# Kernel optimization log

Hardware: AMD Instinct MI355X
Metric: run time of the kernel (lower is better)

The kernel has to match this reference:

```python
import jax, jax.numpy as jnp
import numpy as np

PHI = 0.1  # fraction of pruned weights randomized per inference


def setup_inputs() -> dict:
    key = jax.random.key(0)
    k1, k2, k3 = jax.random.split(key, 3)
    d_out, d_in, batch = 8192, 8192, 256
    W = jax.random.normal(k1, (d_out, d_in), jnp.float32) * 0.02
    prune = jax.random.uniform(k2, (d_out, d_in)) < 0.9
    W = jnp.where(prune, 0.0, W)
    mask = (W == 0.0)  # _register_masks: pruned positions
    x = jax.random.normal(k3, (batch, d_in), jnp.float32)
    return {"x": x, "W": W, "mask": mask}


def reference(x, W, mask):
    # --- _apply_random_flip (vectorized) ---
    n_pruned = int(np.asarray(jnp.sum(mask)))          # concrete mask -> static count
    n_flip = max(1, int(PHI * n_pruned))
    keep = ~mask
    n_keep = jnp.sum(keep).astype(W.dtype)
    wk = jnp.where(keep, W, 0.0)
    mean = jnp.sum(wk) / n_keep
    # torch .std() is unbiased (n-1 denominator)
    var = jnp.sum(jnp.where(keep, (W - mean) ** 2, 0.0)) / (n_keep - 1.0)
    std = jnp.sqrt(var)
    key = jax.random.key(42)
    ks, kv = jax.random.split(key)
    # uniform random permutation of pruned indices -> top_k of random scores
    scores = jnp.where(mask.ravel(), jax.random.uniform(ks, (W.size,)), -1.0)
    _, flip_idx = jax.lax.top_k(scores, n_flip)        # [n_flip] flat indices into W
    vals = jax.random.normal(kv, (n_flip,), W.dtype) * std * 0.1
    W_flipped = W.ravel().at[flip_idx].set(vals).reshape(W.shape)
    # --- base_model forward (Linear, no bias) ---
    out = x @ W_flipped.T                               # [batch, d_out]
    # --- _restore_masks: zero flipped weights again (no effect on out) ---
    _ = jnp.where(mask, 0.0, W_flipped)
    return out
```

## Files before the change

kernel.cpp:

```cpp
#include <hip/hip_runtime.h>

typedef unsigned int u32;
typedef unsigned long long u64;
typedef unsigned short u16;

#define NTOT   67108864u
#define T0P    7399424u
#define PBASE  14452u
#define NSUP   1932u
#define NWSEG  4096u
#define WCAP   2176u
#define RCAP   4352u
#define KSPLIT 8
#define RBLK   512u
#define SEGPB  8

struct Scalars {
  double sumW;
  double sumW2;
  u64 npruned;
  u64 nflip;
  float stdf;
  float pad;
};

#define OFF_COLSUM 0ull
#define OFF_ALLOC  8192ull
#define OFF_SBASE  16384ull
#define OFF_SC     24576ull
#define OFF_SEGCNT 24704ull
#define OFF_BHIST  41216ull
#define OFF_BDEST  4235520ull
#define OFF_XBF    8429824ull
#define OFF_SEGS   12624128ull
#define OFF_ROUTED 48275712ull
#define OFF_WBF    81846400ull
#define WS_NEED_WBF 216064128ull
#define ROUTED_CAP 8388608u
#define OFF_OUTP   OFF_SEGS

__host__ __device__ inline void tf2x32(u32 k0, u32 k1, u32 x0, u32 x1, u32& y0, u32& y1) {
  u32 ks2 = k0 ^ k1 ^ 0x1BD11BDAu;
  x0 += k0; x1 += k1;
#define TFR(r) { x0 += x1; x1 = (x1 << (r)) | (x1 >> (32 - (r))); x1 ^= x0; }
  TFR(13) TFR(15) TFR(26) TFR(6)  x0 += k1;  x1 += ks2 + 1u;
  TFR(17) TFR(29) TFR(16) TFR(24) x0 += ks2; x1 += k0 + 2u;
  TFR(13) TFR(15) TFR(26) TFR(6)  x0 += k0;  x1 += k1 + 3u;
  TFR(17) TFR(29) TFR(16) TFR(24) x0 += k1;  x1 += ks2 + 4u;
  TFR(13) TFR(15) TFR(26) TFR(6)  x0 += ks2; x1 += k0 + 5u;
#undef TFR
  y0 = x0; y1 = x1;
}

__device__ inline u32 jax_bits32(u32 k0, u32 k1, u32 i) {
  u32 y0, y1; tf2x32(k0, k1, 0u, i, y0, y1);
  return y0 ^ y1;
}

__device__ inline u16 f2bf(float f) {
  union { float f; u32 u; } c; c.f = f;
  u32 r = ((c.u >> 16) & 1u) + 0x7FFFu;
  return (u16)((c.u + r) >> 16);
}

__device__ inline float erfinv32(float x) {
  float w = -log1pf(-x * x);
  float p;
  if (w < 5.0f) {
    w -= 2.5f;
    p = 2.81022636e-08f;
    p = fmaf(p, w, 3.43273939e-07f);
    p = fmaf(p, w, -3.5233877e-06f);
    p = fmaf(p, w, -4.39150654e-06f);
    p = fmaf(p, w, 0.00021858087f);
    p = fmaf(p, w, -0.00125372503f);
    p = fmaf(p, w, -0.00417768164f);
    p = fmaf(p, w, 0.246640727f);
    p = fmaf(p, w, 1.50140941f);
  } else {
    w = sqrtf(w) - 3.0f;
    p = -0.000200214257f;
    p = fmaf(p, w, 0.000100950558f);
    p = fmaf(p, w, 0.00134934322f);
    p = fmaf(p, w, -0.00367342844f);
    p = fmaf(p, w, 0.00573950773f);
    p = fmaf(p, w, -0.0076224613f);
    p = fmaf(p, w, 0.00943887047f);
    p = fmaf(p, w, 1.00167406f);
    p = fmaf(p, w, 2.83297682f);
  }
  return p * x;
}

__device__ inline void pass1_half(const float* __restrict__ W, Scalars* sc,
                                  u32* segcnt, u32* segs, u32 uk0, u32 uk1,
                                  u32 bid, u32 t, u32 lo, u32 hi, bool first) {
  u32 gid = bid * 256 + t;
  u32 lane = t & 63;
  u32 wid = gid >> 6;
  u32* wseg = segs + (u64)wid * WCAP;
  u32 wbase = first ? 0u : segcnt[wid];
  float sf = 0.f, sf2 = 0.f; u32 cnt = 0;
  const u32 stride4 = 1024u * 256u * 4u;
  for (u32 b4 = lo + gid * 4; b4 < hi; b4 += stride4) {
    float4 w4 = *(const float4*)(W + b4);
    u32 sb0 = jax_bits32(uk0, uk1, b4 + 0) >> 9;
    u32 sb1 = jax_bits32(uk0, uk1, b4 + 1) >> 9;
    u32 sb2 = jax_bits32(uk0, uk1, b4 + 2) >> 9;
    u32 sb3 = jax_bits32(uk0, uk1, b4 + 3) >> 9;
    float we[4] = {w4.x, w4.y, w4.z, w4.w};
    u32 sbv[4] = {sb0, sb1, sb2, sb3};
    u32 cand[4]; u32 nc = 0;
#pragma unroll
    for (int e = 0; e < 4; e++) {
      float w = we[e];
      sf += w;
      sf2 = fmaf(w, w, sf2);
      bool pr = (w == 0.0f);
      cnt += pr ? 1u : 0u;
      if (pr && sbv[e] >= T0P) { cand[nc] = b4 + e; nc++; }
    }
    u32 inc = nc;
#pragma unroll
    for (int o = 1; o < 64; o <<= 1) { u32 v = (u32)__shfl_up((int)inc, o); if (lane >= (u32)o) inc += v; }
    u32 tot = (u32)__shfl((int)inc, 63);
    u32 pos = wbase + inc - nc;
    for (u32 k2 = 0; k2 < nc; k2++)
      if (pos + k2 < WCAP) wseg[pos + k2] = cand[k2];
    wbase += tot;
  }
  double s = (double)sf, s2 = (double)sf2;
  for (int o = 32; o > 0; o >>= 1) {
    s += __shfl_down(s, o); s2 += __shfl_down(s2, o); cnt += __shfl_down(cnt, o);
  }
  if (lane == 0) {
    atomicAdd(&sc->sumW, s);
    atomicAdd(&sc->sumW2, s2);
    atomicAdd(&sc->npruned, (u64)cnt);
    segcnt[wid] = first ? wbase : ((wbase > WCAP) ? WCAP : wbase);
  }
}

__device__ inline void wconv_range(const float* __restrict__ W, u16* __restrict__ wbf,
                                   u32 i0, u32 glo, u32 ghi) {
  const u32 stride = 512u * 256u;
  for (u32 g = glo + i0; g < ghi; g += stride) {
    const float4* p = (const float4*)(W + (u64)g * 8);
    float4 a = p[0], b = p[1];
    uint4 o;
    o.x = (u32)f2bf(a.x) | ((u32)f2bf(a.y) << 16);
    o.y = (u32)f2bf(a.z) | ((u32)f2bf(a.w) << 16);
    o.z = (u32)f2bf(b.x) | ((u32)f2bf(b.y) << 16);
    o.w = (u32)f2bf(b.z) | ((u32)f2bf(b.w) << 16);
    *(uint4*)(wbf + (u64)g * 8) = o;
  }
}

__global__ __launch_bounds__(256) void k_pass1wA(const float* __restrict__ W,
                                                 u16* __restrict__ wbf,
                                                 const float* __restrict__ x,
                                                 u16* __restrict__ xbf,
                                                 Scalars* sc, u32* segcnt, u32* segs,
                                                 u32 uk0, u32 uk1, u32 dowbf) {
  u32 t = threadIdx.x, bid = blockIdx.x;
  if (bid < 1024u) {
    pass1_half(W, sc, segcnt, segs, uk0, uk1, bid, t, 0u, NTOT / 2u, true);
  } else if (bid < 1536u) {
    if (dowbf) wconv_range(W, wbf, (bid - 1024u) * 256 + t, 0u, NTOT / 16u);
  } else {
    u32 i0 = (bid - 1536u) * 256 + t;
    const u32 stride = 512u * 256u;
    for (u32 g = i0; g < 524288u; g += stride) {
      float4 v = ((const float4*)x)[g];
      ushort4 o; o.x = f2bf(v.x); o.y = f2bf(v.y); o.z = f2bf(v.z); o.w = f2bf(v.w);
      ((ushort4*)xbf)[g] = o;
    }
  }
}

__global__ __launch_bounds__(256) void k_pass1wB(const float* __restrict__ W,
                                                 u16* __restrict__ wbf,
                                                 Scalars* sc, u32* segcnt, u32* segs,
                                                 u32 uk0, u32 uk1) {
  u32 t = threadIdx.x, bid = blockIdx.x;
  if (bid < 1024u) {
    pass1_half(W, sc, segcnt, segs, uk0, uk1, bid, t, NTOT / 2u, NTOT, false);
  } else {
    wconv_range(W, wbf, (bid - 1024u) * 256 + t, NTOT / 16u, NTOT / 8u);
  }
}

__global__ __launch_bounds__(256) void k_route_a(const u32* __restrict__ segs,
                                                 const u32* __restrict__ segcnt,
                                                 u32* bhist, u32 uk0, u32 uk1) {
  __shared__ u32 lhist[2048];
  u32 t = threadIdx.x;
  for (u32 j = t; j < 2048; j += 256) lhist[j] = 0;
  __syncthreads();
#pragma unroll 1
  for (int sg = 0; sg < SEGPB; sg++) {
    u32 wid = blockIdx.x * SEGPB + sg;
    u32 n = segcnt[wid]; if (n > WCAP) n = WCAP;
    const u32* sp = segs + (u64)wid * WCAP;
    for (u32 i = t; i < n; i += 256) {
      u32 sup = (jax_bits32(uk0, uk1, sp[i]) >> 18) - PBASE;
      atomicAdd(&lhist[sup], 1u);
    }
  }
  __syncthreads();
  for (u32 j = t; j < 2048; j += 256) bhist[blockIdx.x * 2048 + j] = lhist[j];
}

__global__ __launch_bounds__(256) void k_colscan(const u32* __restrict__ bhist,
                                                 u32* bdest, u32* colsum) {
  __shared__ u32 wtmp[4];
  u32 s = blockIdx.x, t = threadIdx.x, lane = t & 63, wv = t >> 6;
  u32 v0 = bhist[(t * 2 + 0) * 2048 + s];
  u32 v1 = bhist[(t * 2 + 1) * 2048 + s];
  u32 pr = v0 + v1;
  u32 inc = pr;
#pragma unroll
  for (int o = 1; o < 64; o <<= 1) { u32 x = (u32)__shfl_up((int)inc, o); if (lane >= (u32)o) inc += x; }
  if (lane == 63) wtmp[wv] = inc;
  __syncthreads();
  u32 woff = 0;
  for (u32 w = 0; w < wv; w++) woff += wtmp[w];
  u32 base = woff + inc - pr;
  bdest[(t * 2 + 0) * 2048 + s] = base;
  bdest[(t * 2 + 1) * 2048 + s] = base + v0;
  if (t == 255) colsum[s] = woff + inc;
}

__global__ __launch_bounds__(256) void k_scan(const u32* __restrict__ colsum, Scalars* sc,
                                              u32* alloc, u32* sbase) {
  __shared__ u32 h[2048];
  __shared__ u32 wtmp[4];
  u32 t = threadIdx.x, lane = t & 63, wv = t >> 6;
  for (u32 j = t; j < 2048; j += 256) h[j] = colsum[j];
  __syncthreads();
  {
    u32 a[8]; u32 s8 = 0;
#pragma unroll
    for (int k = 0; k < 8; k++) { a[k] = h[t * 8 + k]; s8 += a[k]; }
    u32 inc = s8;
#pragma unroll
    for (int o = 1; o < 64; o <<= 1) { u32 v = (u32)__shfl_up((int)inc, o); if (lane >= (u32)o) inc += v; }
    if (lane == 63) wtmp[wv] = inc;
    __syncthreads();
    u32 woff = 0; for (u32 w = 0; w < wv; w++) woff += wtmp[w];
    u32 base = woff + inc - s8;
#pragma unroll
    for (int k = 0; k < 8; k++) { alloc[t * 8 + k] = base; base += a[k]; }
    __syncthreads();
  }
  {
    u32 a[8]; u32 s8 = 0;
#pragma unroll
    for (int k = 0; k < 8; k++) { a[k] = h[2047 - (t * 8 + k)]; s8 += a[k]; }
    u32 inc = s8;
#pragma unroll
    for (int o = 1; o < 64; o <<= 1) { u32 v = (u32)__shfl_up((int)inc, o); if (lane >= (u32)o) inc += v; }
    if (lane == 63) wtmp[wv] = inc;
    __syncthreads();
    u32 woff = 0; for (u32 w = 0; w < wv; w++) woff += wtmp[w];
    u32 base = woff + inc - s8;
#pragma unroll
    for (int k = 0; k < 8; k++) { sbase[2047 - (t * 8 + k)] = base; base += a[k]; }
  }
  if (t == 0) {
    double nk = (double)NTOT - (double)sc->npruned;
    double mean = sc->sumW / nk;
    double var = (sc->sumW2 - 2.0 * mean * sc->sumW + nk * mean * mean) / (nk - 1.0);
    sc->stdf = (float)sqrt(var);
    u64 nfi = (u64)(0.1 * (double)sc->npruned);
    if (nfi < 1) nfi = 1;
    sc->nflip = nfi;
  }
}

__global__ __launch_bounds__(256) void k_route_b(const u32* __restrict__ segs,
                                                 const u32* __restrict__ segcnt,
                                                 const u32* __restrict__ alloc,
                                                 const u32* __restrict__ bdest,
                                                 u32* routed, u32 uk0, u32 uk1) {
  __shared__ u32 lcur[2048];
  u32 t = threadIdx.x;
  for (u32 j = t; j < 2048; j += 256) lcur[j] = alloc[j] + bdest[blockIdx.x * 2048 + j];
  __syncthreads();
#pragma unroll 1
  for (int sg = 0; sg < SEGPB; sg++) {
    u32 wid = blockIdx.x * SEGPB + sg;
    u32 n = segcnt[wid]; if (n > WCAP) n = WCAP;
    const u32* sp = segs + (u64)wid * WCAP;
    for (u32 i = t; i < n; i += 256) {
      u32 idx = sp[i];
      u32 sup = (jax_bits32(uk0, uk1, idx) >> 18) - PBASE;
      u32 pos = atomicAdd(&lcur[sup], 1u);
      if (pos < ROUTED_CAP) routed[pos] = idx;
    }
  }
}

__device__ inline void suf512(const u32* cnt, u32* suf, u32* wtmp) {
  u32 t = threadIdx.x, lane = t & 63, wv = t >> 6;
  u32 a0 = cnt[511 - t * 2], a1 = cnt[510 - t * 2];
  u32 s = a0 + a1;
  u32 inc = s;
#pragma unroll
  for (int o = 1; o < 64; o <<= 1) { u32 v = (u32)__shfl_up((int)inc, o); if (lane >= (u32)o) inc += v; }
  if (lane == 63) wtmp[wv] = inc;
  __syncthreads();
  u32 woff = 0;
  for (u32 w = 0; w < wv; w++) woff += wtmp[w];
  u32 base = woff + inc - s;
  suf[511 - t * 2] = base;
  suf[510 - t * 2] = base + a0;
  __syncthreads();
}

template<int MODE>
__global__ __launch_bounds__(256) void k_rank(float* __restrict__ W,
                                              u16* __restrict__ wbf,
                                              const u32* __restrict__ colsum,
                                              const u32* __restrict__ alloc,
                                              const u32* __restrict__ sbase,
                                              const u32* __restrict__ routed,
                                              const Scalars* __restrict__ sc,
                                              u32 uk0, u32 uk1, u32 vk0, u32 vk1) {
  u32 p = blockIdx.x;
  u32 n = colsum[p]; if (n == 0) return;
  if (n > RCAP) n = RCAP;
  u64 nflip = sc->nflip;
  u32 rbase = sbase[p];
  if ((u64)rbase >= nflip) return;
  __shared__ u32 sIdx[RCAP];
  __shared__ u16 sFine[RCAP];
  __shared__ u32 pIdx[RCAP];
  __shared__ u32 hist[512], gbase[512], cur[512], wtmp[4];
  u32 t = threadIdx.x;
  for (u32 j = t; j < 512; j += 256) hist[j] = 0;
  __syncthreads();
  const u32* src = routed + alloc[p];
  for (u32 i = t; i < n; i += 256) {
    u32 idx = src[i];
    u32 f = (jax_bits32(uk0, uk1, idx) >> 9) & 511u;
    sIdx[i] = idx;
    sFine[i] = (u16)f;
    atomicAdd(&hist[f], 1u);
  }
  __syncthreads();
  suf512(hist, gbase, wtmp);
  for (u32 j = t; j < 512; j += 256) cur[j] = gbase[j];
  __syncthreads();
  for (u32 i = t; i < n; i += 256) {
    u32 pos = atomicAdd(&cur[sFine[i]], 1u);
    pIdx[pos] = sIdx[i];
  }
  __syncthreads();
  float stdf = sc->stdf;
  for (u32 i = t; i < n; i += 256) {
    u32 f = sFine[i];
    u32 g0 = gbase[f], g1 = g0 + hist[f];
    u32 v = sIdx[i];
    u32 ord = 0;
    for (u32 q = g0; q < g1; q++) ord += (pIdx[q] < v) ? 1u : 0u;
    u64 rank = (u64)rbase + g0 + ord;
    if (rank >= nflip) continue;
    u32 bits = jax_bits32(vk0, vk1, (u32)rank);
    union { u32 u; float fl; } cv; cv.u = 0x3F800000u | (bits >> 9);
    float fu = cv.fl - 1.0f;
    const float lo = -0.99999994f;
    float u2 = fmaxf(lo, fu * 2.0f + lo);
    float nrm = 1.41421354f * erfinv32(u2);
    float val = (nrm * stdf) * 0.1f;
    if (MODE == 1) wbf[v] = f2bf(val);
    else           W[v] = val;
  }
}

typedef __bf16 bf16x8 __attribute__((ext_vector_type(8)));
typedef float f32x4 __attribute__((ext_vector_type(4)));

__global__ __launch_bounds__(256, 3) void k_gemm2(const u16* __restrict__ xbf,
                                                  const u16* __restrict__ wbf,
                                                  float* __restrict__ outp) {
  __shared__ u16 As[128 * 64];
  __shared__ u16 Bs[128 * 64];
  u32 i = blockIdx.x;
  u32 xcd = i & 7u, slot = i >> 3;
  u32 mi = slot & 1u, qq = slot >> 1;
  u32 pid = xcd * 64u + qq;
  u32 kidx = pid >> 6;
  u32 nb = pid & 63u;
  u32 mrow = mi * 128u, nrow = nb * 128u;
  u32 kbase = kidx * 1024u;
  u32 tid = threadIdx.x;
  u32 lane = tid & 63, wv = tid >> 6;
  u32 l8 = lane & 7;
  u32 lr = lane >> 3;
  u32 wm = wv >> 1, wn = wv & 1;
  u32 r = lane & 15, q = lane >> 4;
  f32x4 acc[4][4];
#pragma unroll
  for (int a = 0; a < 4; a++)
#pragma unroll
    for (int b = 0; b < 4; b++) acc[a][b] = (f32x4){0.f, 0.f, 0.f, 0.f};

  for (u32 kb = kbase; kb < kbase + 1024u; kb += 64u) {
#pragma unroll
    for (int j = 0; j < 4; j++) {
      u32 g = wv * 4 + (u32)j;
      u32 row = g * 8 + lr;
      u32 sc = ((l8 ^ (row & 7u)) * 8u);
      const u16* ga = xbf + (u64)(mrow + row) * 8192 + kb + sc;
      __builtin_amdgcn_global_load_lds((const u32*)ga, (u32*)&As[g * 512u], 16, 0, 0);
      const u16* gb = wbf + (u64)(nrow + row) * 8192 + kb + sc;
      __builtin_amdgcn_global_load_lds((const u32*)gb, (u32*)&Bs[g * 512u], 16, 0, 0);
    }
    __syncthreads();
#pragma unroll
    for (int ks = 0; ks < 2; ks++) {
      bf16x8 a[4], b[4];
      u32 ch = (u32)(ks * 4) + q;
#pragma unroll
      for (int mt = 0; mt < 4; mt++) {
        u32 row = wm * 64 + (u32)mt * 16 + r;
        a[mt] = *(bf16x8*)&As[row * 64 + ((ch ^ (r & 7u)) * 8u)];
      }
#pragma unroll
      for (int nt = 0; nt < 4; nt++) {
        u32 row = wn * 64 + (u32)nt * 16 + r;
        b[nt] = *(bf16x8*)&Bs[row * 64 + ((ch ^ (r & 7u)) * 8u)];
      }
#pragma unroll
      for (int mt = 0; mt < 4; mt++)
#pragma unroll
        for (int nt = 0; nt < 4; nt++)
          acc[mt][nt] = __builtin_amdgcn_mfma_f32_16x16x32_bf16(a[mt], b[nt], acc[mt][nt], 0, 0, 0);
    }
    __syncthreads();
  }
  float* op = outp + (u64)kidx * 2097152u;
  u32 quad = lane >> 4, col = lane & 15;
#pragma unroll
  for (int mt = 0; mt < 4; mt++)
#pragma unroll
    for (int nt = 0; nt < 4; nt++) {
      u32 n = nrow + wn * 64 + (u32)nt * 16 + col;
#pragma unroll
      for (int rg = 0; rg < 4; rg++) {
        u32 m = mrow + wm * 64 + (u32)mt * 16 + quad * 4 + (u32)rg;
        op[(u64)m * 8192 + n] = acc[mt][nt][rg];
      }
    }
}

__global__ __launch_bounds__(256) void k_redout(const float* __restrict__ part,
                                                float* __restrict__ out) {
  u32 i = blockIdx.x * 256 + threadIdx.x;
  float4 s = ((const float4*)part)[i];
#pragma unroll
  for (int k = 1; k < KSPLIT; k++) {
    float4 v = ((const float4*)(part + (u64)k * 2097152u))[i];
    s.x += v.x; s.y += v.y; s.z += v.z; s.w += v.w;
  }
  ((float4*)out)[i] = s;
}

__global__ __launch_bounds__(256, 2) void k_gemm_fb(const u16* __restrict__ xbf,
                                                    const float* __restrict__ W,
                                                    float* __restrict__ out) {
  __shared__ u16 xs[256 * 72];
  __shared__ u16 wsm[64 * 72];
  u32 tid = threadIdx.x;
  u32 lane = tid & 63, wv = tid >> 6;
  u32 nt0 = blockIdx.x * 64;
  u32 kbase = blockIdx.y * 2048u;
  f32x4 acc[4][4];
#pragma unroll
  for (int i = 0; i < 4; i++)
#pragma unroll
    for (int j = 0; j < 4; j++) acc[i][j] = (f32x4){0.f, 0.f, 0.f, 0.f};
  for (u32 kb = kbase; kb < kbase + 2048u; kb += 64u) {
#pragma unroll
    for (int r8 = 0; r8 < 8; r8++) {
      u32 row = r8 * 32 + (tid >> 3);
      u32 kseg = (tid & 7) * 8;
      uint4 v = *(const uint4*)(xbf + (u64)row * 8192 + kb + kseg);
      *(uint4*)&xs[row * 72 + kseg] = v;
    }
#pragma unroll
    for (int rr = 0; rr < 4; rr++) {
      u32 f4 = rr * 256 + tid;
      u32 row = f4 >> 4;
      u32 kc = (f4 & 15) * 4;
      float4 v = *(const float4*)(W + (u64)(nt0 + row) * 8192 + kb + kc);
      ushort4 o; o.x = f2bf(v.x); o.y = f2bf(v.y); o.z = f2bf(v.z); o.w = f2bf(v.w);
      *(ushort4*)&wsm[row * 72 + kc] = o;
    }
    __syncthreads();
#pragma unroll
    for (int ks = 0; ks < 2; ks++) {
      bf16x8 a[4], b[4];
      u32 koff = ks * 32 + (lane >> 4) * 8;
      u32 rsel = lane & 15;
#pragma unroll
      for (int mt = 0; mt < 4; mt++) a[mt] = *(bf16x8*)&xs[(wv * 64 + mt * 16 + rsel) * 72 + koff];
#pragma unroll
      for (int nt = 0; nt < 4; nt++) b[nt] = *(bf16x8*)&wsm[(nt * 16 + rsel) * 72 + koff];
#pragma unroll
      for (int mt = 0; mt < 4; mt++)
#pragma unroll
        for (int nt = 0; nt < 4; nt++)
          acc[mt][nt] = __builtin_amdgcn_mfma_f32_16x16x32_bf16(a[mt], b[nt], acc[mt][nt], 0, 0, 0);
    }
    __syncthreads();
  }
  u32 quad = lane >> 4, col = lane & 15;
#pragma unroll
  for (int mt = 0; mt < 4; mt++)
#pragma unroll
    for (int nt = 0; nt < 4; nt++) {
      u32 n = nt0 + nt * 16 + col;
#pragma unroll
      for (int rg = 0; rg < 4; rg++) {
        u32 m = wv * 64 + mt * 16 + quad * 4 + rg;
        atomicAdd(&out[(u64)m * 8192 + n], acc[mt][nt][rg]);
      }
    }
}

extern "C" void kernel_launch(void* const* d_in, const int* in_sizes, int n_in,
                              void* d_out, int out_size, void* d_ws, size_t ws_size,
                              hipStream_t stream) {
  const float* x; float* W;
  if (in_sizes[0] == 2097152) { x = (const float*)d_in[0]; W = (float*)d_in[1]; }
  else                        { x = (const float*)d_in[1]; W = (float*)d_in[0]; }
  float* out = (float*)d_out;
  char* ws = (char*)d_ws;

  u32* colsum = (u32*)(ws + OFF_COLSUM);
  u32* alloc  = (u32*)(ws + OFF_ALLOC);
  u32* sbase  = (u32*)(ws + OFF_SBASE);
  Scalars* sc = (Scalars*)(ws + OFF_SC);
  u32* segcnt = (u32*)(ws + OFF_SEGCNT);
  u32* bhist  = (u32*)(ws + OFF_BHIST);
  u32* bdest  = (u32*)(ws + OFF_BDEST);
  u16* xbf    = (u16*)(ws + OFF_XBF);
  u32* segs   = (u32*)(ws + OFF_SEGS);
  u32* routed = (u32*)(ws + OFF_ROUTED);
  u16* wbf    = (u16*)(ws + OFF_WBF);
  float* outp = (float*)(ws + OFF_OUTP);

  bool t1 = (ws_size >= (size_t)WS_NEED_WBF);

  u32 a0, a1, b0, b1;
  tf2x32(0u, 42u, 0u, 0u, a0, a1);
  tf2x32(0u, 42u, 0u, 1u, b0, b1);

  hipMemsetAsync(sc, 0, sizeof(Scalars), stream);

  k_pass1wA<<<2048, 256, 0, stream>>>(W, wbf, x, xbf, sc, segcnt, segs, a0, a1, t1 ? 1u : 0u);
  k_pass1wB<<<t1 ? 1536 : 1024, 256, 0, stream>>>(W, wbf, sc, segcnt, segs, a0, a1);
  k_route_a<<<RBLK, 256, 0, stream>>>(segs, segcnt, bhist, a0, a1);
  k_colscan<<<2048, 256, 0, stream>>>(bhist, bdest, colsum);
  k_scan<<<1, 256, 0, stream>>>(colsum, sc, alloc, sbase);
  k_route_b<<<RBLK, 256, 0, stream>>>(segs, segcnt, alloc, bdest, routed, a0, a1);
  if (t1) {
    k_rank<1><<<NSUP, 256, 0, stream>>>(W, wbf, colsum, alloc, sbase, routed, sc, a0, a1, b0, b1);
    k_gemm2<<<1024, 256, 0, stream>>>(xbf, wbf, outp);
    k_redout<<<2048, 256, 0, stream>>>(outp, out);
  } else {
    k_rank<0><<<NSUP, 256, 0, stream>>>(W, wbf, colsum, alloc, sbase, routed, sc, a0, a1, b0, b1);
    hipMemsetAsync(out, 0, (size_t)out_size * 4, stream);
    dim3 g(128, 4);
    k_gemm_fb<<<g, 256, 0, stream>>>(xbf, W, out);
  }
}
```

Before: 1.134 ms.

## Fuse routing, scan and rank stages into one cooperative persistent kernel

The five middle kernels (histogram, column scan, global scan, scatter route, rank/flip) are merged into a single cooperative kernel of 768 blocks that uses grid-wide syncs between phases, with a shared-memory union covering all phases. The two-pass weight statistics/conversion kernels are also merged into one launch over the full array, with the bf16 conversion given more blocks. The aim is to remove launch gaps and tail effects between many short dependent kernels. The cost is grid-sync overhead and fewer blocks working on the rank phase, where each block now loops over several super-buckets.

```diff
diff --git a/kernel.cpp b/kernel.cpp
--- a/kernel.cpp
+++ b/kernel.cpp
@@ -1,4 +1,7 @@
 #include <hip/hip_runtime.h>
+#include <hip/hip_cooperative_groups.h>
+
+namespace cg = cooperative_groups;
 
 typedef unsigned int u32;
 typedef unsigned long long u64;
@@ -12,8 +15,7 @@
 #define WCAP   2176u
 #define RCAP   4352u
 #define KSPLIT 8
-#define RBLK   512u
-#define SEGPB  8
+#define MBLK   768u
 
 struct Scalars {
   double sumW;
@@ -30,12 +32,12 @@
 #define OFF_SC     24576ull
 #define OFF_SEGCNT 24704ull
 #define OFF_BHIST  41216ull
-#define OFF_BDEST  4235520ull
-#define OFF_XBF    8429824ull
-#define OFF_SEGS   12624128ull
-#define OFF_ROUTED 48275712ull
-#define OFF_WBF    81846400ull
-#define WS_NEED_WBF 216064128ull
+#define OFF_BDEST  8429824ull
+#define OFF_XBF    16818432ull
+#define OFF_SEGS   21012736ull
+#define OFF_ROUTED 56664320ull
+#define OFF_WBF    90218752ull
+#define WS_NEED_WBF 224436480ull
 #define ROUTED_CAP 8388608u
 #define OFF_OUTP   OFF_SEGS
 
@@ -92,84 +94,76 @@
   return p * x;
 }
 
-__device__ inline void pass1_half(const float* __restrict__ W, Scalars* sc,
-                                  u32* segcnt, u32* segs, u32 uk0, u32 uk1,
-                                  u32 bid, u32 t, u32 lo, u32 hi, bool first) {
-  u32 gid = bid * 256 + t;
-  u32 lane = t & 63;
-  u32 wid = gid >> 6;
-  u32* wseg = segs + (u64)wid * WCAP;
-  u32 wbase = first ? 0u : segcnt[wid];
-  float sf = 0.f, sf2 = 0.f; u32 cnt = 0;
-  const u32 stride4 = 1024u * 256u * 4u;
-  for (u32 b4 = lo + gid * 4; b4 < hi; b4 += stride4) {
-    float4 w4 = *(const float4*)(W + b4);
-    u32 sb0 = jax_bits32(uk0, uk1, b4 + 0) >> 9;
-    u32 sb1 = jax_bits32(uk0, uk1, b4 + 1) >> 9;
-    u32 sb2 = jax_bits32(uk0, uk1, b4 + 2) >> 9;
-    u32 sb3 = jax_bits32(uk0, uk1, b4 + 3) >> 9;
-    float we[4] = {w4.x, w4.y, w4.z, w4.w};
-    u32 sbv[4] = {sb0, sb1, sb2, sb3};
-    u32 cand[4]; u32 nc = 0;
-#pragma unroll
-    for (int e = 0; e < 4; e++) {
-      float w = we[e];
-      sf += w;
-      sf2 = fmaf(w, w, sf2);
-      bool pr = (w == 0.0f);
-      cnt += pr ? 1u : 0u;
-      if (pr && sbv[e] >= T0P) { cand[nc] = b4 + e; nc++; }
-    }
-    u32 inc = nc;
-#pragma unroll
-    for (int o = 1; o < 64; o <<= 1) { u32 v = (u32)__shfl_up((int)inc, o); if (lane >= (u32)o) inc += v; }
-    u32 tot = (u32)__shfl((int)inc, 63);
-    u32 pos = wbase + inc - nc;
-    for (u32 k2 = 0; k2 < nc; k2++)
-      if (pos + k2 < WCAP) wseg[pos + k2] = cand[k2];
-    wbase += tot;
-  }
-  double s = (double)sf, s2 = (double)sf2;
-  for (int o = 32; o > 0; o >>= 1) {
-    s += __shfl_down(s, o); s2 += __shfl_down(s2, o); cnt += __shfl_down(cnt, o);
-  }
-  if (lane == 0) {
-    atomicAdd(&sc->sumW, s);
-    atomicAdd(&sc->sumW2, s2);
-    atomicAdd(&sc->npruned, (u64)cnt);
-    segcnt[wid] = first ? wbase : ((wbase > WCAP) ? WCAP : wbase);
-  }
-}
-
-__device__ inline void wconv_range(const float* __restrict__ W, u16* __restrict__ wbf,
-                                   u32 i0, u32 glo, u32 ghi) {
-  const u32 stride = 512u * 256u;
-  for (u32 g = glo + i0; g < ghi; g += stride) {
-    const float4* p = (const float4*)(W + (u64)g * 8);
-    float4 a = p[0], b = p[1];
-    uint4 o;
-    o.x = (u32)f2bf(a.x) | ((u32)f2bf(a.y) << 16);
-    o.y = (u32)f2bf(a.z) | ((u32)f2bf(a.w) << 16);
-    o.z = (u32)f2bf(b.x) | ((u32)f2bf(b.y) << 16);
-    o.w = (u32)f2bf(b.z) | ((u32)f2bf(b.w) << 16);
-    *(uint4*)(wbf + (u64)g * 8) = o;
-  }
-}
-
-__global__ __launch_bounds__(256) void k_pass1wA(const float* __restrict__ W,
-                                                 u16* __restrict__ wbf,
-                                                 const float* __restrict__ x,
-                                                 u16* __restrict__ xbf,
-                                                 Scalars* sc, u32* segcnt, u32* segs,
-                                                 u32 uk0, u32 uk1, u32 dowbf) {
-  u32 t = threadIdx.x, bid = blockIdx.x;
+__global__ __launch_bounds__(256) void k_pass1w(const float* __restrict__ W,
+                                                u16* __restrict__ wbf,
+                                                const float* __restrict__ x,
+                                                u16* __restrict__ xbf,
+                                                Scalars* sc, u32* segcnt, u32* segs,
+                                                u32 uk0, u32 uk1, u32 dowbf) {
+  u32 t = threadIdx.x;
+  u32 bid = blockIdx.x;
   if (bid < 1024u) {
-    pass1_half(W, sc, segcnt, segs, uk0, uk1, bid, t, 0u, NTOT / 2u, true);
-  } else if (bid < 1536u) {
-    if (dowbf) wconv_range(W, wbf, (bid - 1024u) * 256 + t, 0u, NTOT / 16u);
+    u32 gid = bid * 256 + t;
+    u32 lane = t & 63;
+    u32 wid = gid >> 6;
+    u32* wseg = segs + (u64)wid * WCAP;
+    u32 wbase = 0;
+    float sf = 0.f, sf2 = 0.f; u32 cnt = 0;
+    const u32 stride4 = 1024u * 256u * 4u;
+    for (u32 b4 = gid * 4; b4 < NTOT; b4 += stride4) {
+      float4 w4 = *(const float4*)(W + b4);
+      u32 sb0 = jax_bits32(uk0, uk1, b4 + 0) >> 9;
+      u32 sb1 = jax_bits32(uk0, uk1, b4 + 1) >> 9;
+      u32 sb2 = jax_bits32(uk0, uk1, b4 + 2) >> 9;
+      u32 sb3 = jax_bits32(uk0, uk1, b4 + 3) >> 9;
+      float we[4] = {w4.x, w4.y, w4.z, w4.w};
+      u32 sbv[4] = {sb0, sb1, sb2, sb3};
+      u32 cand[4]; u32 nc = 0;
+#pragma unroll
+      for (int e = 0; e < 4; e++) {
+        float w = we[e];
+        sf += w;
+        sf2 = fmaf(w, w, sf2);
+        bool pr = (w == 0.0f);
+        cnt += pr ? 1u : 0u;
+        if (pr && sbv[e] >= T0P) { cand[nc] = b4 + e; nc++; }
+      }
+      u32 inc = nc;
+#pragma unroll
+      for (int o = 1; o < 64; o <<= 1) { u32 v = (u32)__shfl_up((int)inc, o); if (lane >= (u32)o) inc += v; }
+      u32 tot = (u32)__shfl((int)inc, 63);
+      u32 pos = wbase + inc - nc;
+      for (u32 k2 = 0; k2 < nc; k2++)
+        if (pos + k2 < WCAP) wseg[pos + k2] = cand[k2];
+      wbase += tot;
+    }
+    double s = (double)sf, s2 = (double)sf2;
+    for (int o = 32; o > 0; o >>= 1) {
+      s += __shfl_down(s, o); s2 += __shfl_down(s2, o); cnt += __shfl_down(cnt, o);
+    }
+    if (lane == 0) {
+      atomicAdd(&sc->sumW, s);
+      atomicAdd(&sc->sumW2, s2);
+      atomicAdd(&sc->npruned, (u64)cnt);
+      segcnt[wid] = (wbase > WCAP) ? WCAP : wbase;
+    }
+  } else if (bid < 1984u) {
+    if (!dowbf) return;
+    u32 i0 = (bid - 1024u) * 256 + t;
+    const u32 stride = 960u * 256u;
+    for (u32 g = i0; g < NTOT / 8u; g += stride) {
+      const float4* p = (const float4*)(W + (u64)g * 8);
+      float4 a = p[0], b = p[1];
+      uint4 o;
+      o.x = (u32)f2bf(a.x) | ((u32)f2bf(a.y) << 16);
+      o.y = (u32)f2bf(a.z) | ((u32)f2bf(a.w) << 16);
+      o.z = (u32)f2bf(b.x) | ((u32)f2bf(b.y) << 16);
+      o.w = (u32)f2bf(b.z) | ((u32)f2bf(b.w) << 16);
+      *(uint4*)(wbf + (u64)g * 8) = o;
+    }
   } else {
-    u32 i0 = (bid - 1536u) * 256 + t;
-    const u32 stride = 512u * 256u;
+    u32 i0 = (bid - 1984u) * 256 + t;
+    const u32 stride = 64u * 256u;
     for (u32 g = i0; g < 524288u; g += stride) {
       float4 v = ((const float4*)x)[g];
       ushort4 o; o.x = f2bf(v.x); o.y = f2bf(v.y); o.z = f2bf(v.z); o.w = f2bf(v.w);
@@ -178,128 +172,13 @@
   }
 }
 
-__global__ __launch_bounds__(256) void k_pass1wB(const float* __restrict__ W,
-                                                 u16* __restrict__ wbf,
-                                                 Scalars* sc, u32* segcnt, u32* segs,
-                                                 u32 uk0, u32 uk1) {
-  u32 t = threadIdx.x, bid = blockIdx.x;
-  if (bid < 1024u) {
-    pass1_half(W, sc, segcnt, segs, uk0, uk1, bid, t, NTOT / 2u, NTOT, false);
-  } else {
-    wconv_range(W, wbf, (bid - 1024u) * 256 + t, NTOT / 16u, NTOT / 8u);
-  }
-}
-
-__global__ __launch_bounds__(256) void k_route_a(const u32* __restrict__ segs,
-                                                 const u32* __restrict__ segcnt,
-                                                 u32* bhist, u32 uk0, u32 uk1) {
-  __shared__ u32 lhist[2048];
-  u32 t = threadIdx.x;
-  for (u32 j = t; j < 2048; j += 256) lhist[j] = 0;
-  __syncthreads();
-#pragma unroll 1
-  for (int sg = 0; sg < SEGPB; sg++) {
-    u32 wid = blockIdx.x * SEGPB + sg;
-    u32 n = segcnt[wid]; if (n > WCAP) n = WCAP;
-    const u32* sp = segs + (u64)wid * WCAP;
-    for (u32 i = t; i < n; i += 256) {
-      u32 sup = (jax_bits32(uk0, uk1, sp[i]) >> 18) - PBASE;
-      atomicAdd(&lhist[sup], 1u);
-    }
-  }
-  __syncthreads();
-  for (u32 j = t; j < 2048; j += 256) bhist[blockIdx.x * 2048 + j] = lhist[j];
-}
-
-__global__ __launch_bounds__(256) void k_colscan(const u32* __restrict__ bhist,
-                                                 u32* bdest, u32* colsum) {
-  __shared__ u32 wtmp[4];
-  u32 s = blockIdx.x, t = threadIdx.x, lane = t & 63, wv = t >> 6;
-  u32 v0 = bhist[(t * 2 + 0) * 2048 + s];
-  u32 v1 = bhist[(t * 2 + 1) * 2048 + s];
-  u32 pr = v0 + v1;
-  u32 inc = pr;
-#pragma unroll
-  for (int o = 1; o < 64; o <<= 1) { u32 x = (u32)__shfl_up((int)inc, o); if (lane >= (u32)o) inc += x; }
-  if (lane == 63) wtmp[wv] = inc;
-  __syncthreads();
-  u32 woff = 0;
-  for (u32 w = 0; w < wv; w++) woff += wtmp[w];
-  u32 base = woff + inc - pr;
-  bdest[(t * 2 + 0) * 2048 + s] = base;
-  bdest[(t * 2 + 1) * 2048 + s] = base + v0;
-  if (t == 255) colsum[s] = woff + inc;
-}
-
-__global__ __launch_bounds__(256) void k_scan(const u32* __restrict__ colsum, Scalars* sc,
-                                              u32* alloc, u32* sbase) {
-  __shared__ u32 h[2048];
-  __shared__ u32 wtmp[4];
-  u32 t = threadIdx.x, lane = t & 63, wv = t >> 6;
-  for (u32 j = t; j < 2048; j += 256) h[j] = colsum[j];
-  __syncthreads();
-  {
-    u32 a[8]; u32 s8 = 0;
-#pragma unroll
-    for (int k = 0; k < 8; k++) { a[k] = h[t * 8 + k]; s8 += a[k]; }
-    u32 inc = s8;
-#pragma unroll
-    for (int o = 1; o < 64; o <<= 1) { u32 v = (u32)__shfl_up((int)inc, o); if (lane >= (u32)o) inc += v; }
-    if (lane == 63) wtmp[wv] = inc;
-    __syncthreads();
-    u32 woff = 0; for (u32 w = 0; w < wv; w++) woff += wtmp[w];
-    u32 base = woff + inc - s8;
-#pragma unroll
-    for (int k = 0; k < 8; k++) { alloc[t * 8 + k] = base; base += a[k]; }
-    __syncthreads();
-  }
-  {
-    u32 a[8]; u32 s8 = 0;
-#pragma unroll
-    for (int k = 0; k < 8; k++) { a[k] = h[2047 - (t * 8 + k)]; s8 += a[k]; }
-    u32 inc = s8;
-#pragma unroll
-    for (int o = 1; o < 64; o <<= 1) { u32 v = (u32)__shfl_up((int)inc, o); if (lane >= (u32)o) inc += v; }
-    if (lane == 63) wtmp[wv] = inc;
-    __syncthreads();
-    u32 woff = 0; for (u32 w = 0; w < wv; w++) woff += wtmp[w];
-    u32 base = woff + inc - s8;
-#pragma unroll
-    for (int k = 0; k < 8; k++) { sbase[2047 - (t * 8 + k)] = base; base += a[k]; }
-  }
-  if (t == 0) {
-    double nk = (double)NTOT - (double)sc->npruned;
-    double mean = sc->sumW / nk;
-    double var = (sc->sumW2 - 2.0 * mean * sc->sumW + nk * mean * mean) / (nk - 1.0);
-    sc->stdf = (float)sqrt(var);
-    u64 nfi = (u64)(0.1 * (double)sc->npruned);
-    if (nfi < 1) nfi = 1;
-    sc->nflip = nfi;
-  }
-}
-
-__global__ __launch_bounds__(256) void k_route_b(const u32* __restrict__ segs,
-                                                 const u32* __restrict__ segcnt,
-                                                 const u32* __restrict__ alloc,
-                                                 const u32* __restrict__ bdest,
-                                                 u32* routed, u32 uk0, u32 uk1) {
-  __shared__ u32 lcur[2048];
-  u32 t = threadIdx.x;
-  for (u32 j = t; j < 2048; j += 256) lcur[j] = alloc[j] + bdest[blockIdx.x * 2048 + j];
-  __syncthreads();
-#pragma unroll 1
-  for (int sg = 0; sg < SEGPB; sg++) {
-    u32 wid = blockIdx.x * SEGPB + sg;
-    u32 n = segcnt[wid]; if (n > WCAP) n = WCAP;
-    const u32* sp = segs + (u64)wid * WCAP;
-    for (u32 i = t; i < n; i += 256) {
-      u32 idx = sp[i];
-      u32 sup = (jax_bits32(uk0, uk1, idx) >> 18) - PBASE;
-      u32 pos = atomicAdd(&lcur[sup], 1u);
-      if (pos < ROUTED_CAP) routed[pos] = idx;
-    }
-  }
-}
+union MidLds {
+  struct { u32 lhist[2048]; } ra;
+  struct { u32 wt[4]; } cb;
+  struct { u32 h[2048]; u32 wt[4]; } cs;
+  struct { u32 lcur[2048]; } rb;
+  struct { u32 pIdx[RCAP]; u16 sFine[RCAP]; u32 hist[512]; u32 gbase[512]; u32 cur[512]; u32 wt[4]; } rk;
+};
 
 __device__ inline void suf512(const u32* cnt, u32* suf, u32* wtmp) {
   u32 t = threadIdx.x, lane = t & 63, wv = t >> 6;
@@ -319,62 +198,152 @@
 }
 
 template<int MODE>
-__global__ __launch_bounds__(256) void k_rank(float* __restrict__ W,
-                                              u16* __restrict__ wbf,
-                                              const u32* __restrict__ colsum,
-                                              const u32* __restrict__ alloc,
-                                              const u32* __restrict__ sbase,
-                                              const u32* __restrict__ routed,
-                                              const Scalars* __restrict__ sc,
-                                              u32 uk0, u32 uk1, u32 vk0, u32 vk1) {
-  u32 p = blockIdx.x;
-  u32 n = colsum[p]; if (n == 0) return;
-  if (n > RCAP) n = RCAP;
+__global__ __launch_bounds__(256, 3) void k_mid(const u32* __restrict__ segs,
+                                                const u32* __restrict__ segcnt,
+                                                u32* bhist, u32* bdest,
+                                                u32* colsum, u32* alloc, u32* sbase,
+                                                Scalars* sc, u32* routed,
+                                                float* W, u16* wbf,
+                                                u32 uk0, u32 uk1, u32 vk0, u32 vk1) {
+  cg::grid_group grid = cg::this_grid();
+  __shared__ MidLds u;
+  u32 bid = blockIdx.x, t = threadIdx.x, lane = t & 63, wv = t >> 6;
+
+  for (u32 j = t; j < 2048; j += 256) u.ra.lhist[j] = 0;
+  __syncthreads();
+  for (u32 wid = bid; wid < NWSEG; wid += MBLK) {
+    u32 n = segcnt[wid]; if (n > WCAP) n = WCAP;
+    const u32* sp = segs + (u64)wid * WCAP;
+    for (u32 i = t; i < n; i += 256) {
+      u32 sup = (jax_bits32(uk0, uk1, sp[i]) >> 18) - PBASE;
+      atomicAdd(&u.ra.lhist[sup], 1u);
+    }
+  }
+  __syncthreads();
+  for (u32 j = t; j < 2048; j += 256) bhist[bid * 2048 + j] = u.ra.lhist[j];
+  grid.sync();
+
+  for (u32 s = bid; s < 2048u; s += MBLK) {
+    u32 aa[3]; u32 ssum = 0;
+#pragma unroll
+    for (int k = 0; k < 3; k++) { aa[k] = bhist[(t * 3 + (u32)k) * 2048 + s]; ssum += aa[k]; }
+    u32 inc = ssum;
+#pragma unroll
+    for (int o = 1; o < 64; o <<= 1) { u32 v = (u32)__shfl_up((int)inc, o); if (lane >= (u32)o) inc += v; }
+    if (lane == 63) u.cb.wt[wv] = inc;
+    __syncthreads();
+    u32 woff = 0;
+    for (u32 w = 0; w < wv; w++) woff += u.cb.wt[w];
+    u32 base = woff + inc - ssum;
+#pragma unroll
+    for (int k = 0; k < 3; k++) { bdest[(t * 3 + (u32)k) * 2048 + s] = base; base += aa[k]; }
+    if (t == 255) colsum[s] = woff + inc;
+    __syncthreads();
+  }
+  grid.sync();
+
+  if (bid == 0) {
+    for (u32 j = t; j < 2048; j += 256) u.cs.h[j] = colsum[j];
+    __syncthreads();
+    {
+      u32 a[8]; u32 s8 = 0;
+#pragma unroll
+      for (int k = 0; k < 8; k++) { a[k] = u.cs.h[t * 8 + k]; s8 += a[k]; }
+      u32 inc = s8;
+#pragma unroll
+      for (int o = 1; o < 64; o <<= 1) { u32 v = (u32)__shfl_up((int)inc, o); if (lane >= (u32)o) inc += v; }
+      if (lane == 63) u.cs.wt[wv] = inc;
+      __syncthreads();
+      u32 woff = 0; for (u32 w = 0; w < wv; w++) woff += u.cs.wt[w];
+      u32 base = woff + inc - s8;
+#pragma unroll
+      for (int k = 0; k < 8; k++) { alloc[t * 8 + k] = base; base += a[k]; }
+      __syncthreads();
+    }
+    {
+      u32 a[8]; u32 s8 = 0;
+#pragma unroll
+      for (int k = 0; k < 8; k++) { a[k] = u.cs.h[2047 - (t * 8 + k)]; s8 += a[k]; }
+      u32 inc = s8;
+#pragma unroll
+      for (int o = 1; o < 64; o <<= 1) { u32 v = (u32)__shfl_up((int)inc, o); if (lane >= (u32)o) inc += v; }
+      if (lane == 63) u.cs.wt[wv] = inc;
+      __syncthreads();
+      u32 woff = 0; for (u32 w = 0; w < wv; w++) woff += u.cs.wt[w];
+      u32 base = woff + inc - s8;
+#pragma unroll
+      for (int k = 0; k < 8; k++) { sbase[2047 - (t * 8 + k)] = base; base += a[k]; }
+    }
+    if (t == 0) {
+      double nk = (double)NTOT - (double)sc->npruned;
+      double mean = sc->sumW / nk;
+      double var = (sc->sumW2 - 2.0 * mean * sc->sumW + nk * mean * mean) / (nk - 1.0);
+      sc->stdf = (float)sqrt(var);
+      u64 nfi = (u64)(0.1 * (double)sc->npruned);
+      if (nfi < 1) nfi = 1;
+      sc->nflip = nfi;
+    }
+  }
+  grid.sync();
+
+  for (u32 j = t; j < 2048; j += 256) u.rb.lcur[j] = alloc[j] + bdest[bid * 2048 + j];
+  __syncthreads();
+  for (u32 wid = bid; wid < NWSEG; wid += MBLK) {
+    u32 n = segcnt[wid]; if (n > WCAP) n = WCAP;
+    const u32* sp = segs + (u64)wid * WCAP;
+    for (u32 i = t; i < n; i += 256) {
+      u32 idx = sp[i];
+      u32 sup = (jax_bits32(uk0, uk1, idx) >> 18) - PBASE;
+      u32 pos = atomicAdd(&u.rb.lcur[sup], 1u);
+      if (pos < ROUTED_CAP) routed[pos] = idx;
+    }
+  }
+  grid.sync();
+
   u64 nflip = sc->nflip;
-  u32 rbase = sbase[p];
-  if ((u64)rbase >= nflip) return;
-  __shared__ u32 sIdx[RCAP];
-  __shared__ u16 sFine[RCAP];
-  __shared__ u32 pIdx[RCAP];
-  __shared__ u32 hist[512], gbase[512], cur[512], wtmp[4];
-  u32 t = threadIdx.x;
-  for (u32 j = t; j < 512; j += 256) hist[j] = 0;
-  __syncthreads();
-  const u32* src = routed + alloc[p];
-  for (u32 i = t; i < n; i += 256) {
-    u32 idx = src[i];
-    u32 f = (jax_bits32(uk0, uk1, idx) >> 9) & 511u;
-    sIdx[i] = idx;
-    sFine[i] = (u16)f;
-    atomicAdd(&hist[f], 1u);
-  }
-  __syncthreads();
-  suf512(hist, gbase, wtmp);
-  for (u32 j = t; j < 512; j += 256) cur[j] = gbase[j];
-  __syncthreads();
-  for (u32 i = t; i < n; i += 256) {
-    u32 pos = atomicAdd(&cur[sFine[i]], 1u);
-    pIdx[pos] = sIdx[i];
-  }
-  __syncthreads();
   float stdf = sc->stdf;
-  for (u32 i = t; i < n; i += 256) {
-    u32 f = sFine[i];
-    u32 g0 = gbase[f], g1 = g0 + hist[f];
-    u32 v = sIdx[i];
-    u32 ord = 0;
-    for (u32 q = g0; q < g1; q++) ord += (pIdx[q] < v) ? 1u : 0u;
-    u64 rank = (u64)rbase + g0 + ord;
-    if (rank >= nflip) continue;
-    u32 bits = jax_bits32(vk0, vk1, (u32)rank);
-    union { u32 u; float fl; } cv; cv.u = 0x3F800000u | (bits >> 9);
-    float fu = cv.fl - 1.0f;
-    const float lo = -0.99999994f;
-    float u2 = fmaxf(lo, fu * 2.0f + lo);
-    float nrm = 1.41421354f * erfinv32(u2);
-    float val = (nrm * stdf) * 0.1f;
-    if (MODE == 1) wbf[v] = f2bf(val);
-    else           W[v] = val;
+  for (u32 p = bid; p < NSUP; p += MBLK) {
+    u32 n = colsum[p]; if (n == 0) continue;
+    if (n > RCAP) n = RCAP;
+    u32 rbase = sbase[p];
+    if ((u64)rbase >= nflip) continue;
+    __syncthreads();
+    for (u32 j = t; j < 512; j += 256) u.rk.hist[j] = 0;
+    __syncthreads();
+    const u32* src = routed + alloc[p];
+    for (u32 i = t; i < n; i += 256) {
+      u32 f = (jax_bits32(uk0, uk1, src[i]) >> 9) & 511u;
+      u.rk.sFine[i] = (u16)f;
+      atomicAdd(&u.rk.hist[f], 1u);
+    }
+    __syncthreads();
+    suf512(u.rk.hist, u.rk.gbase, u.rk.wt);
+    for (u32 j = t; j < 512; j += 256) u.rk.cur[j] = u.rk.gbase[j];
+    __syncthreads();
+    for (u32 i = t; i < n; i += 256) {
+      u32 pos = atomicAdd(&u.rk.cur[u.rk.sFine[i]], 1u);
+      u.rk.pIdx[pos] = src[i];
+    }
+    __syncthreads();
+    for (u32 i = t; i < n; i += 256) {
+      u32 f = u.rk.sFine[i];
+      u32 g0 = u.rk.gbase[f], g1 = g0 + u.rk.hist[f];
+      u32 v = src[i];
+      u32 ord = 0;
+      for (u32 q = g0; q < g1; q++) ord += (u.rk.pIdx[q] < v) ? 1u : 0u;
+      u64 rank = (u64)rbase + g0 + ord;
+      if (rank >= nflip) continue;
+      u32 bits = jax_bits32(vk0, vk1, (u32)rank);
+      union { u32 u; float fl; } cv; cv.u = 0x3F800000u | (bits >> 9);
+      float fu = cv.fl - 1.0f;
+      const float lo = -0.99999994f;
+      float u2 = fmaxf(lo, fu * 2.0f + lo);
+      float nrm = 1.41421354f * erfinv32(u2);
+      float val = (nrm * stdf) * 0.1f;
+      if (MODE == 1) wbf[v] = f2bf(val);
+      else           W[v] = val;
+    }
+    __syncthreads();
   }
 }
 
@@ -560,18 +529,19 @@
 
   hipMemsetAsync(sc, 0, sizeof(Scalars), stream);
 
-  k_pass1wA<<<2048, 256, 0, stream>>>(W, wbf, x, xbf, sc, segcnt, segs, a0, a1, t1 ? 1u : 0u);
-  k_pass1wB<<<t1 ? 1536 : 1024, 256, 0, stream>>>(W, wbf, sc, segcnt, segs, a0, a1);
-  k_route_a<<<RBLK, 256, 0, stream>>>(segs, segcnt, bhist, a0, a1);
-  k_colscan<<<2048, 256, 0, stream>>>(bhist, bdest, colsum);
-  k_scan<<<1, 256, 0, stream>>>(colsum, sc, alloc, sbase);
-  k_route_b<<<RBLK, 256, 0, stream>>>(segs, segcnt, alloc, bdest, routed, a0, a1);
+  u32 dowbf = t1 ? 1u : 0u;
+  k_pass1w<<<2048, 256, 0, stream>>>(W, wbf, x, xbf, sc, segcnt, segs, a0, a1, dowbf);
+
+  void* margs[] = {(void*)&segs, (void*)&segcnt, (void*)&bhist, (void*)&bdest,
+                   (void*)&colsum, (void*)&alloc, (void*)&sbase, (void*)&sc,
+                   (void*)&routed, (void*)&W, (void*)&wbf,
+                   (void*)&a0, (void*)&a1, (void*)&b0, (void*)&b1};
   if (t1) {
-    k_rank<1><<<NSUP, 256, 0, stream>>>(W, wbf, colsum, alloc, sbase, routed, sc, a0, a1, b0, b1);
+    hipLaunchCooperativeKernel((void*)&k_mid<1>, dim3(MBLK), dim3(256), margs, 0, stream);
     k_gemm2<<<1024, 256, 0, stream>>>(xbf, wbf, outp);
     k_redout<<<2048, 256, 0, stream>>>(outp, out);
   } else {
-    k_rank<0><<<NSUP, 256, 0, stream>>>(W, wbf, colsum, alloc, sbase, routed, sc, a0, a1, b0, b1);
+    hipLaunchCooperativeKernel((void*)&k_mid<0>, dim3(MBLK), dim3(256), margs, 0, stream);
     hipMemsetAsync(out, 0, (size_t)out_size * 4, stream);
     dim3 g(128, 4);
     k_gemm_fb<<<g, 256, 0, stream>>>(xbf, W, out);
```

Result: slower. 1.407 ms (+24.1%).
